# Optimization experiments

Hardware: AMD Instinct MI355X
Metric: run time of the kernel (lower is better)

The kernel has to match this reference:

```python
import math
import jax, jax.numpy as jnp
import numpy as np

D, NH, NL, NP = 256, 8, 4, 4
C = D // NH
VALUE_SHAPES = np.array([[128, 128], [64, 64], [32, 32], [16, 16]], dtype=np.int32)


def _offset_bias():
    # Faithful to MSDeformAttn._reset_parameters grid init for sampling_offsets.bias
    th = np.arange(NH, dtype=np.float32) * (2.0 * np.pi / NH)
    g = np.stack([np.cos(th), np.sin(th)], -1)                      # [NH,2]
    g = g / np.abs(g).max(-1, keepdims=True)
    g = np.tile(g[:, None, None, :], (1, NL, NP, 1))                # [NH,NL,NP,2]
    g = g * np.arange(1, NP + 1, dtype=np.float32)[None, None, :, None]
    return jnp.asarray(g.reshape(-1), jnp.float32)


def setup_inputs() -> dict:
    key = jax.random.key(0)
    ks = jax.random.split(key, 10)
    bs, Q = 8, 2048
    LV = int((VALUE_SHAPES[:, 0] * VALUE_SHAPES[:, 1]).sum())
    s = 0.02
    return {
        "query": jax.random.normal(ks[0], (bs, Q, D), jnp.float32),
        "refer_bbox": jax.random.uniform(ks[1], (bs, Q, NL, 2), jnp.float32),
        "value": jax.random.normal(ks[2], (bs, LV, D), jnp.float32),
        "value_shapes": VALUE_SHAPES,  # static numpy (shapes must be compile-time constants)
        "W_value": jax.random.normal(ks[3], (D, D), jnp.float32) * s,
        "b_value": jnp.zeros((D,), jnp.float32),
        "W_off": jax.random.normal(ks[4], (D, NH * NL * NP * 2), jnp.float32) * 0.01,
        "b_off": _offset_bias(),
        "W_attn": jax.random.normal(ks[5], (D, NH * NL * NP), jnp.float32) * s,
        "b_attn": jnp.zeros((NH * NL * NP,), jnp.float32),
        "W_out": jax.random.normal(ks[6], (D, D), jnp.float32) * s,
        "b_out": jnp.zeros((D,), jnp.float32),
    }


def _ms_deform_attn(value, shapes, loc, attn):
    # value: [bs,LV,NH,C], loc: [bs,Q,NH,NL,NP,2] in [0,1], attn: [bs,Q,NH,NL,NP]
    bs, LV = value.shape[:2]
    Q = loc.shape[1]
    BH = bs * NH
    v = value.transpose(0, 2, 1, 3).reshape(BH, LV, C)              # [BH,LV,C]
    loc = loc.transpose(0, 2, 1, 3, 4, 5).reshape(BH, Q, NL, NP, 2)
    attn = attn.transpose(0, 2, 1, 3, 4).reshape(BH, Q, NL, NP)
    acc = jnp.zeros((BH, Q, C), value.dtype)
    start = 0
    for lvl in range(NL):
        H, W = int(shapes[lvl, 0]), int(shapes[lvl, 1])
        img = v[:, start:start + H * W]                             # [BH,HW,C]
        start += H * W
        # grid_sample(align_corners=False): pixel coord = loc * size - 0.5
        x = loc[:, :, lvl, :, 0] * W - 0.5                          # [BH,Q,NP]
        y = loc[:, :, lvl, :, 1] * H - 0.5
        x0 = jnp.floor(x); y0 = jnp.floor(y)
        fx = x - x0; fy = y - y0
        x0i = x0.astype(jnp.int32); y0i = y0.astype(jnp.int32)
        samp = jnp.zeros((BH, Q, NP, C), value.dtype)
        for dx, dy in ((0, 0), (1, 0), (0, 1), (1, 1)):
            xi = x0i + dx; yi = y0i + dy
            valid = (xi >= 0) & (xi < W) & (yi >= 0) & (yi < H)     # zero padding
            w = (fx if dx else 1.0 - fx) * (fy if dy else 1.0 - fy)
            w = jnp.where(valid, w, 0.0)
            idx = jnp.clip(yi, 0, H - 1) * W + jnp.clip(xi, 0, W - 1)
            g = jnp.take_along_axis(img, idx.reshape(BH, Q * NP)[..., None], axis=1)
            samp = samp + w[..., None] * g.reshape(BH, Q, NP, C)
        acc = acc + (samp * attn[:, :, lvl, :, None]).sum(2)
    return acc.reshape(bs, NH, Q, C).transpose(0, 2, 1, 3).reshape(bs, Q, D)


def reference(query, refer_bbox, value, value_shapes, W_value, b_value,
              W_off, b_off, W_attn, b_attn, W_out, b_out):
    shapes = np.asarray(value_shapes)  # static
    bs, Q = query.shape[:2]
    LV = value.shape[1]
    v = (value @ W_value + b_value).reshape(bs, LV, NH, C)
    off = (query @ W_off + b_off).reshape(bs, Q, NH, NL, NP, 2)
    attn = jax.nn.softmax((query @ W_attn + b_attn).reshape(bs, Q, NH, NL * NP), -1)
    attn = attn.reshape(bs, Q, NH, NL, NP)
    norm = jnp.asarray(shapes[:, ::-1], query.dtype)                # (W,H) per level
    loc = refer_bbox[:, :, None, :, None, :] + off / norm[None, None, None, :, None, :]
    out = _ms_deform_attn(v, shapes, loc, attn)
    return out @ W_out + b_out
```

## Files before the change

kernel.cpp:

```cpp
#include <hip/hip_runtime.h>
#include <hip/hip_bf16.h>

#define D_MODEL 256
#define NHEAD   8
#define NLVL    4
#define NPTS    4
#define CH      32
#define QTOT    2048
#define BS      8
#define LVTOT   21760
#define KDIM    256

typedef __attribute__((ext_vector_type(8))) short bf16x8;
typedef __attribute__((ext_vector_type(4))) float f32x4;

__device__ inline float bf_lo(unsigned u) { unsigned t = u << 16; float f; __builtin_memcpy(&f, &t, 4); return f; }
__device__ inline float bf_hi(unsigned u) { unsigned t = u & 0xffff0000u; float f; __builtin_memcpy(&f, &t, 4); return f; }
__device__ inline float bfu2f(unsigned short s) { unsigned t = (unsigned)s << 16; float f; __builtin_memcpy(&f, &t, 4); return f; }
__device__ inline unsigned short f2bfu(float f) { __hip_bfloat16 h = __float2bfloat16(f); unsigned short u; __builtin_memcpy(&u, &h, 2); return u; }

#define BK  64
#define LDP 72
#define LDC2 136

__device__ inline void transpose_W_body(const float* __restrict__ W,
                                        __hip_bfloat16* __restrict__ Wt,
                                        int sh, int blk, int tid) {
    int t = blk * 256 + tid;
    int k = t >> sh, n = t & ((1 << sh) - 1);
    Wt[n * 256 + k] = __float2bfloat16(W[(k << sh) + n]);
}

__global__ __launch_bounds__(256)
void convert_all(const float* __restrict__ q, __hip_bfloat16* __restrict__ qb,
                 const float* __restrict__ Wv, __hip_bfloat16* __restrict__ Wtv,
                 const float* __restrict__ Wo, __hip_bfloat16* __restrict__ Wto,
                 const float* __restrict__ Wa, __hip_bfloat16* __restrict__ Wta) {
    const int bid = blockIdx.x;
    const int tid = threadIdx.x;
    if (bid < 4096) {
        int t = bid * 256 + tid;
        float4 f = ((const float4*)q)[t];
        __hip_bfloat16 h4[4] = {__float2bfloat16(f.x), __float2bfloat16(f.y),
                                __float2bfloat16(f.z), __float2bfloat16(f.w)};
        ((uint2*)qb)[t] = *(const uint2*)h4;
    } else if (bid < 4352) {
        transpose_W_body(Wv, Wtv, 8, bid - 4096, tid);
    } else if (bid < 4608) {
        transpose_W_body(Wo, Wto, 8, bid - 4352, tid);
    } else {
        transpose_W_body(Wa, Wta, 7, bid - 4608, tid);
    }
}

__global__ __launch_bounds__(256)
void convert_W(const float* __restrict__ W, __hip_bfloat16* __restrict__ Wt, int sh) {
    int t = blockIdx.x * 256 + threadIdx.x;
    int k = t >> sh, n = t & ((1 << sh) - 1);
    Wt[n * 256 + k] = __float2bfloat16(W[(k << sh) + n]);
}

__device__ void value_gemm_body(char* smem, int bid_v,
                                const float* __restrict__ A,
                                const __hip_bfloat16* __restrict__ Wt,
                                const float* __restrict__ bias,
                                __hip_bfloat16* __restrict__ v) {
    __hip_bfloat16* As = (__hip_bfloat16*)smem;
    __hip_bfloat16* Bs = (__hip_bfloat16*)(smem + 128 * LDP * 2);
    __hip_bfloat16* Cs = (__hip_bfloat16*)smem;

    const int tid  = threadIdx.x;
    const int lane = tid & 63;
    const int wave = tid >> 6;
    const int wr   = wave >> 1;
    const int wc   = wave & 1;
    const int cb      = (bid_v & 1) * 128;
    const int rowBase = (bid_v >> 1) * 128;

    const int m0   = lane & 15;
    const int quad = lane >> 4;

    const int ar = tid >> 4;
    const int ac = tid & 15;
    const int br = tid >> 3;
    const int bc = tid & 7;

    f32x4 acc[4][4] = {};

    for (int kc = 0; kc < KDIM; kc += BK) {
#pragma unroll
        for (int i = 0; i < 8; ++i) {
            const int row = i * 16 + ar;
            float4 f = *(const float4*)(A + (size_t)(rowBase + row) * KDIM + kc + ac * 4);
            __hip_bfloat16 t4[4] = {__float2bfloat16(f.x), __float2bfloat16(f.y),
                                    __float2bfloat16(f.z), __float2bfloat16(f.w)};
            *(uint2*)&As[row * LDP + ac * 4] = *(const uint2*)t4;
        }
#pragma unroll
        for (int i = 0; i < 4; ++i) {
            const int row = i * 32 + br;
            uint4 u = *(const uint4*)(Wt + (size_t)(cb + row) * KDIM + kc + bc * 8);
            *(uint4*)&Bs[row * LDP + bc * 8] = u;
        }
        __syncthreads();

#pragma unroll
        for (int ks = 0; ks < 2; ++ks) {
            bf16x8 af[4], bfv[4];
#pragma unroll
            for (int i = 0; i < 4; ++i)
                af[i] = *(const bf16x8*)&As[(wr * 64 + i * 16 + m0) * LDP + ks * 32 + quad * 8];
#pragma unroll
            for (int j = 0; j < 4; ++j)
                bfv[j] = *(const bf16x8*)&Bs[(wc * 64 + j * 16 + m0) * LDP + ks * 32 + quad * 8];
#pragma unroll
            for (int i = 0; i < 4; ++i)
#pragma unroll
                for (int j = 0; j < 4; ++j)
                    acc[i][j] = __builtin_amdgcn_mfma_f32_16x16x32_bf16(af[i], bfv[j], acc[i][j], 0, 0, 0);
        }
        __syncthreads();
    }

    const int b = rowBase / LVTOT;
    const int pixBase = rowBase - b * LVTOT;
#pragma unroll
    for (int half = 0; half < 2; ++half) {
        if (wr == half) {
#pragma unroll
            for (int j = 0; j < 4; ++j) {
                const int lcol = wc * 64 + j * 16 + m0;
                const float bv = bias[cb + lcol];
#pragma unroll
                for (int i = 0; i < 4; ++i) {
                    const int lrow = i * 16 + quad * 4;
#pragma unroll
                    for (int r = 0; r < 4; ++r)
                        Cs[(lrow + r) * LDC2 + lcol] = __float2bfloat16(acc[i][j][r] + bv);
                }
            }
        }
        __syncthreads();
        char* dst = (char*)v + (size_t)(b * LVTOT + pixBase + half * 64) * 512 + cb * 2;
        const char* src = (const char*)Cs;
#pragma unroll
        for (int itr = 0; itr < 4; ++itr) {
            const int o = itr * 4096 + tid * 16;
            const int row = o >> 8;
            const int c   = o & 255;
            uint4 val = *(const uint4*)(src + row * (LDC2 * 2) + c);
            *(uint4*)(dst + (size_t)row * 512 + c) = val;
        }
        if (half == 0) __syncthreads();
    }
}

__device__ void offattn_gemm_body(char* smem, int bid,
                                  const __hip_bfloat16* __restrict__ A,
                                  const __hip_bfloat16* __restrict__ Wt_oa,
                                  const float* __restrict__ b_off,
                                  const float* __restrict__ b_attn,
                                  float* __restrict__ off_ws,
                                  float* __restrict__ logits_ws) {
    __hip_bfloat16* As = (__hip_bfloat16*)smem;
    __hip_bfloat16* Bs = (__hip_bfloat16*)(smem + 128 * LDP * 2);

    const int tid  = threadIdx.x;
    const int lane = tid & 63;
    const int wave = tid >> 6;
    const int rowBase = (bid & 127) * 128;
    const int cb      = (bid >> 7) * 128;

    const int m0   = lane & 15;
    const int quad = lane >> 4;

    const int br = tid >> 3;
    const int bc = tid & 7;

    f32x4 acc[2][8] = {};

    for (int kc = 0; kc < KDIM; kc += BK) {
#pragma unroll
        for (int i = 0; i < 4; ++i) {
            const int row = i * 32 + br;
            uint4 ua = *(const uint4*)(A     + (size_t)(rowBase + row) * KDIM + kc + bc * 8);
            uint4 ub = *(const uint4*)(Wt_oa + (size_t)(cb + row) * KDIM + kc + bc * 8);
            *(uint4*)&As[row * LDP + bc * 8] = ua;
            *(uint4*)&Bs[row * LDP + bc * 8] = ub;
        }
        __syncthreads();

#pragma unroll
        for (int ks = 0; ks < 2; ++ks) {
            bf16x8 af[2], bfv[8];
#pragma unroll
            for (int i = 0; i < 2; ++i)
                af[i] = *(const bf16x8*)&As[(wave * 32 + i * 16 + m0) * LDP + ks * 32 + quad * 8];
#pragma unroll
            for (int j = 0; j < 8; ++j)
                bfv[j] = *(const bf16x8*)&Bs[(j * 16 + m0) * LDP + ks * 32 + quad * 8];
#pragma unroll
            for (int i = 0; i < 2; ++i)
#pragma unroll
                for (int j = 0; j < 8; ++j)
                    acc[i][j] = __builtin_amdgcn_mfma_f32_16x16x32_bf16(af[i], bfv[j], acc[i][j], 0, 0, 0);
        }
        __syncthreads();
    }

#pragma unroll
    for (int j = 0; j < 8; ++j) {
        const int col = cb + j * 16 + m0;
        const bool isOff = (col < 256);
        const float bv = isOff ? b_off[col] : b_attn[col - 256];
#pragma unroll
        for (int i = 0; i < 2; ++i) {
            const int row0 = rowBase + wave * 32 + i * 16 + quad * 4;
#pragma unroll
            for (int r = 0; r < 4; ++r) {
                const float val = acc[i][j][r] + bv;
                if (isOff) off_ws[(size_t)(row0 + r) * 256 + col] = val;
                else       logits_ws[(size_t)(row0 + r) * 128 + (col - 256)] = val;
            }
        }
    }
}

__global__ __launch_bounds__(256, 2)
void fused_gemms(const float* __restrict__ value,
                 const __hip_bfloat16* __restrict__ Wt_v,
                 const float* __restrict__ b_value,
                 __hip_bfloat16* __restrict__ v_ws,
                 const __hip_bfloat16* __restrict__ q_bf,
                 const __hip_bfloat16* __restrict__ Wt_oa,
                 const float* __restrict__ b_off,
                 const float* __restrict__ b_attn,
                 float* __restrict__ off_ws,
                 float* __restrict__ logits_ws) {
    __shared__ __align__(16) char smem[36864];
    const int bid = blockIdx.x;
    if (bid < 384) {
        offattn_gemm_body(smem, bid, q_bf, Wt_oa, b_off, b_attn, off_ws, logits_ws);
    } else {
        value_gemm_body(smem, bid - 384, value, Wt_v, b_value, v_ws);
    }
}

struct StorePlain {
    float* o;
    int ncol;
    __device__ void operator()(int row, int col, float val) const {
        o[(size_t)row * ncol + col] = val;
    }
};

template <typename Store>
__global__ __launch_bounds__(256, 2)
void gemm_bf16_mfma(const __hip_bfloat16* __restrict__ A,
                    const __hip_bfloat16* __restrict__ Wt,
                    const float* __restrict__ bias, Store store) {
    __shared__ __align__(16) __hip_bfloat16 As[128 * LDP];
    __shared__ __align__(16) __hip_bfloat16 Bs[128 * LDP];

    const int tid  = threadIdx.x;
    const int lane = tid & 63;
    const int wave = tid >> 6;
    const int rowBase = blockIdx.x * 128;
    const int cb = blockIdx.y * 128;

    const int m0   = lane & 15;
    const int quad = lane >> 4;

    const int br = tid >> 3;
    const int bc = tid & 7;

    f32x4 acc[2][8] = {};

    for (int kc = 0; kc < KDIM; kc += BK) {
#pragma unroll
        for (int i = 0; i < 4; ++i) {
            const int row = i * 32 + br;
            uint4 ua = *(const uint4*)(A  + (size_t)(rowBase + row) * KDIM + kc + bc * 8);
            uint4 ub = *(const uint4*)(Wt + (size_t)(cb + row) * KDIM + kc + bc * 8);
            *(uint4*)&As[row * LDP + bc * 8] = ua;
            *(uint4*)&Bs[row * LDP + bc * 8] = ub;
        }
        __syncthreads();

#pragma unroll
        for (int ks = 0; ks < 2; ++ks) {
            bf16x8 af[2], bfv[8];
#pragma unroll
            for (int i = 0; i < 2; ++i)
                af[i] = *(const bf16x8*)&As[(wave * 32 + i * 16 + m0) * LDP + ks * 32 + quad * 8];
#pragma unroll
            for (int j = 0; j < 8; ++j)
                bfv[j] = *(const bf16x8*)&Bs[(j * 16 + m0) * LDP + ks * 32 + quad * 8];
#pragma unroll
            for (int i = 0; i < 2; ++i)
#pragma unroll
                for (int j = 0; j < 8; ++j)
                    acc[i][j] = __builtin_amdgcn_mfma_f32_16x16x32_bf16(af[i], bfv[j], acc[i][j], 0, 0, 0);
        }
        __syncthreads();
    }

#pragma unroll
    for (int j = 0; j < 8; ++j) {
        const int col = cb + j * 16 + m0;
        const float bv = bias[col];
#pragma unroll
        for (int i = 0; i < 2; ++i) {
            const int row0 = rowBase + wave * 32 + i * 16 + quad * 4;
#pragma unroll
            for (int r = 0; r < 4; ++r)
                store(row0 + r, col, acc[i][j][r] + bv);
        }
    }
}

__global__ __launch_bounds__(256)
void sample_kernel(const float* __restrict__ off_ws,
                   const float* __restrict__ logits_ws,
                   const float* __restrict__ bbox,
                   const __hip_bfloat16* __restrict__ v,
                   __hip_bfloat16* __restrict__ acc_bf) {
    __shared__ __align__(16) float off_s[8 * 256];
    __shared__ __align__(16) float attn_s[8 * 128];
    __shared__ float bbox_s[64];
    __shared__ __align__(16) int idx_s[1024 * 4];
    __shared__ __align__(8) unsigned short w_s[1024 * 4];

    const int tid = threadIdx.x;
    const int b = blockIdx.x & 7;
    const int gq0 = b * QTOT + (blockIdx.x >> 3) * 8;

    const float4* osrc = (const float4*)(off_ws + (size_t)gq0 * 256);
    ((float4*)off_s)[tid] = osrc[tid];
    ((float4*)off_s)[tid + 256] = osrc[tid + 256];
    const float4* lsrc = (const float4*)(logits_ws + (size_t)gq0 * 128);
    ((float4*)attn_s)[tid] = lsrc[tid];
    if (tid < 64) bbox_s[tid] = bbox[(size_t)gq0 * 8 + tid];
    __syncthreads();

    if (tid < 64) {
        int qq = tid >> 3, h = tid & 7;
        float* p = attn_s + qq * 128 + h * 16;
        float m = p[0];
#pragma unroll
        for (int i = 1; i < 16; ++i) m = fmaxf(m, p[i]);
        float e[16], s = 0.f;
#pragma unroll
        for (int i = 0; i < 16; ++i) { e[i] = __expf(p[i] - m); s += e[i]; }
        float inv = 1.f / s;
#pragma unroll
        for (int i = 0; i < 16; ++i) p[i] = e[i] * inv;
    }
    __syncthreads();

#pragma unroll
    for (int r = 0; r < 4; ++r) {
        const int tap = tid + r * 256;
        const int qq = tap >> 7, h = (tap >> 4) & 7, l = (tap >> 2) & 3, p = tap & 3;
        const int Wd = 128 >> l;
        const int st = (l == 0) ? 0 : (l == 1) ? 16384 : (l == 2) ? 20480 : 21504;

        const float bx = bbox_s[qq * 8 + l * 2 + 0];
        const float by = bbox_s[qq * 8 + l * 2 + 1];
        const float ox = off_s[qq * 256 + h * 32 + l * 8 + p * 2 + 0];
        const float oy = off_s[qq * 256 + h * 32 + l * 8 + p * 2 + 1];
        const float att = attn_s[qq * 128 + h * 16 + l * 4 + p];

        const float x = bx * (float)Wd + ox - 0.5f;
        const float y = by * (float)Wd + oy - 0.5f;
        const float x0f = floorf(x), y0f = floorf(y);
        const float fx = x - x0f, fy = y - y0f;
        const int x0 = (int)x0f, y0 = (int)y0f;
        const int x1 = x0 + 1, y1 = y0 + 1;
        const bool vx0 = (unsigned)x0 < (unsigned)Wd;
        const bool vx1 = (unsigned)x1 < (unsigned)Wd;
        const bool vy0 = (unsigned)y0 < (unsigned)Wd;
        const bool vy1 = (unsigned)y1 < (unsigned)Wd;
        const int cx0 = min(max(x0, 0), Wd - 1), cx1 = min(max(x1, 0), Wd - 1);
        const int cy0 = min(max(y0, 0), Wd - 1), cy1 = min(max(y1, 0), Wd - 1);

        int4 idx;
        idx.x = (st + cy0 * Wd + cx0) << 9;
        idx.y = (st + cy0 * Wd + cx1) << 9;
        idx.z = (st + cy1 * Wd + cx0) << 9;
        idx.w = (st + cy1 * Wd + cx1) << 9;
        float w0 = (vx0 && vy0) ? (1.f - fx) * (1.f - fy) * att : 0.f;
        float w1 = (vx1 && vy0) ? fx * (1.f - fy) * att : 0.f;
        float w2 = (vx0 && vy1) ? (1.f - fx) * fy * att : 0.f;
        float w3 = (vx1 && vy1) ? fx * fy * att : 0.f;

        *(int4*)&idx_s[tap * 4] = idx;
        unsigned short w4[4] = {f2bfu(w0), f2bfu(w1), f2bfu(w2), f2bfu(w3)};
        *(uint2*)&w_s[tap * 4] = *(const uint2*)w4;
    }
    __syncthreads();

    const int lane = tid & 63;
    const int wave = tid >> 6;
    const int g = lane >> 4;
    const int c2 = lane & 15;

    const char* vbase = (const char*)v + (size_t)b * LVTOT * 512 + c2 * 4;

    for (int i = 0; i < 16; ++i) {
        const int pair = wave * 16 + i;
        const int qq = pair >> 3, hh = pair & 7;
        const char* slab = vbase + hh * 64;
        const int tbase = qq * 128 + hh * 16;

        float ax0 = 0.f, ay0 = 0.f, ax1 = 0.f, ay1 = 0.f, ax2 = 0.f, ay2 = 0.f, ax3 = 0.f, ay3 = 0.f;
#pragma unroll
        for (int ts = 0; ts < 4; ++ts) {
            const int tap = tbase + ts * 4 + g;
            const int4 idx = *(const int4*)&idx_s[tap * 4];
            const ushort4 ww = *(const ushort4*)&w_s[tap * 4];
            unsigned u0 = *(const unsigned*)(slab + idx.x);
            unsigned u1 = *(const unsigned*)(slab + idx.y);
            unsigned u2 = *(const unsigned*)(slab + idx.z);
            unsigned u3 = *(const unsigned*)(slab + idx.w);
            float w0 = bfu2f(ww.x), w1 = bfu2f(ww.y), w2 = bfu2f(ww.z), w3 = bfu2f(ww.w);
            ax0 += w0 * bf_lo(u0); ay0 += w0 * bf_hi(u0);
            ax1 += w1 * bf_lo(u1); ay1 += w1 * bf_hi(u1);
            ax2 += w2 * bf_lo(u2); ay2 += w2 * bf_hi(u2);
            ax3 += w3 * bf_lo(u3); ay3 += w3 * bf_hi(u3);
        }
        float sx = (ax0 + ax1) + (ax2 + ax3);
        float sy = (ay0 + ay1) + (ay2 + ay3);
        sx += __shfl_xor(sx, 16); sy += __shfl_xor(sy, 16);
        sx += __shfl_xor(sx, 32); sy += __shfl_xor(sy, 32);
        if (g == 0) {
            __hip_bfloat16 h2[2] = {__float2bfloat16(sx), __float2bfloat16(sy)};
            unsigned packed; __builtin_memcpy(&packed, h2, 4);
            *(unsigned*)((char*)acc_bf + ((size_t)(gq0 + qq) * 256 + hh * 32 + c2 * 2) * 2) = packed;
        }
    }
}

extern "C" void kernel_launch(void* const* d_in, const int* in_sizes, int n_in,
                              void* d_out, int out_size, void* d_ws, size_t ws_size,
                              hipStream_t stream) {
    const float* query   = (const float*)d_in[0];
    const float* bbox    = (const float*)d_in[1];
    const float* value   = (const float*)d_in[2];
    const float* W_value = (const float*)d_in[4];
    const float* b_value = (const float*)d_in[5];
    const float* W_off   = (const float*)d_in[6];
    const float* b_off   = (const float*)d_in[7];
    const float* W_attn  = (const float*)d_in[8];
    const float* b_attn  = (const float*)d_in[9];
    const float* W_out   = (const float*)d_in[10];
    const float* b_out   = (const float*)d_in[11];
    float* out = (float*)d_out;

    char* ws = (char*)d_ws;
    __hip_bfloat16* v_ws  = (__hip_bfloat16*)ws;
    float* off_ws         = (float*)(ws + 89128960);
    float* logits_ws      = (float*)(ws + 89128960 + 16777216);
    __hip_bfloat16* acc_bf = (__hip_bfloat16*)(ws + 89128960 + 16777216 + 8388608);
    __hip_bfloat16* q_bf   = (__hip_bfloat16*)(ws + 89128960 + 16777216 + 8388608 + 8388608);

    __hip_bfloat16* Wt_v    = acc_bf;
    __hip_bfloat16* Wt_off  = acc_bf + 65536;
    __hip_bfloat16* Wt_attn = acc_bf + 131072;
    __hip_bfloat16* Wt_out  = q_bf;

    const int NQ = BS * QTOT;
    const int NVROWS = BS * LVTOT;

    convert_all<<<4736, 256, 0, stream>>>(query, q_bf,
                                          W_value, Wt_v,
                                          W_off, Wt_off,
                                          W_attn, Wt_attn);

    fused_gemms<<<384 + 2 * (NVROWS / 128), 256, 0, stream>>>(
        value, Wt_v, b_value, v_ws,
        q_bf, Wt_off, b_off, b_attn, off_ws, logits_ws);

    convert_W<<<256, 256, 0, stream>>>(W_out, Wt_out, 8);

    sample_kernel<<<NQ / 8, 256, 0, stream>>>(off_ws, logits_ws, bbox, v_ws, acc_bf);

    gemm_bf16_mfma<<<dim3(NQ / 128, 2), 256, 0, stream>>>(
        acc_bf, Wt_out, b_out, StorePlain{out, 256});
}
```

Before: 390.5 us.

## Widen sample gathers to 8-byte loads, compress indices to u16, process two pairs per iteration

In the sampling kernel, each lane now handles four channels with 8-byte gathers instead of two channels with 4-byte gathers. Eight lanes cover a head's 32 channels and eight lane groups cover the 16 taps, so each iteration processes two (query, head) pairs and keeps 16 gathers in flight. Sample indices are stored as 16-bit row indices in shared memory to halve LDS use, and launch bounds request five blocks per CU for occupancy. The cost is more registers per thread, a three-stage shuffle reduction, and relying on LVTOT fitting in 16 bits.

```diff
diff --git a/kernel.cpp b/kernel.cpp
--- a/kernel.cpp
+++ b/kernel.cpp
@@ -319,7 +319,7 @@
     }
 }
 
-__global__ __launch_bounds__(256)
+__global__ __launch_bounds__(256, 5)
 void sample_kernel(const float* __restrict__ off_ws,
                    const float* __restrict__ logits_ws,
                    const float* __restrict__ bbox,
@@ -328,7 +328,7 @@
     __shared__ __align__(16) float off_s[8 * 256];
     __shared__ __align__(16) float attn_s[8 * 128];
     __shared__ float bbox_s[64];
-    __shared__ __align__(16) int idx_s[1024 * 4];
+    __shared__ __align__(8) unsigned short idx_s[1024 * 4];
     __shared__ __align__(8) unsigned short w_s[1024 * 4];
 
     const int tid = threadIdx.x;
@@ -384,17 +384,17 @@
         const int cx0 = min(max(x0, 0), Wd - 1), cx1 = min(max(x1, 0), Wd - 1);
         const int cy0 = min(max(y0, 0), Wd - 1), cy1 = min(max(y1, 0), Wd - 1);
 
-        int4 idx;
-        idx.x = (st + cy0 * Wd + cx0) << 9;
-        idx.y = (st + cy0 * Wd + cx1) << 9;
-        idx.z = (st + cy1 * Wd + cx0) << 9;
-        idx.w = (st + cy1 * Wd + cx1) << 9;
+        unsigned short pi[4];
+        pi[0] = (unsigned short)(st + cy0 * Wd + cx0);
+        pi[1] = (unsigned short)(st + cy0 * Wd + cx1);
+        pi[2] = (unsigned short)(st + cy1 * Wd + cx0);
+        pi[3] = (unsigned short)(st + cy1 * Wd + cx1);
         float w0 = (vx0 && vy0) ? (1.f - fx) * (1.f - fy) * att : 0.f;
         float w1 = (vx1 && vy0) ? fx * (1.f - fy) * att : 0.f;
         float w2 = (vx0 && vy1) ? (1.f - fx) * fy * att : 0.f;
         float w3 = (vx1 && vy1) ? fx * fy * att : 0.f;
 
-        *(int4*)&idx_s[tap * 4] = idx;
+        *(uint2*)&idx_s[tap * 4] = *(const uint2*)pi;
         unsigned short w4[4] = {f2bfu(w0), f2bfu(w1), f2bfu(w2), f2bfu(w3)};
         *(uint2*)&w_s[tap * 4] = *(const uint2*)w4;
     }
@@ -402,41 +402,91 @@
 
     const int lane = tid & 63;
     const int wave = tid >> 6;
-    const int g = lane >> 4;
-    const int c2 = lane & 15;
-
-    const char* vbase = (const char*)v + (size_t)b * LVTOT * 512 + c2 * 4;
-
-    for (int i = 0; i < 16; ++i) {
-        const int pair = wave * 16 + i;
-        const int qq = pair >> 3, hh = pair & 7;
-        const char* slab = vbase + hh * 64;
-        const int tbase = qq * 128 + hh * 16;
-
-        float ax0 = 0.f, ay0 = 0.f, ax1 = 0.f, ay1 = 0.f, ax2 = 0.f, ay2 = 0.f, ax3 = 0.f, ay3 = 0.f;
-#pragma unroll
-        for (int ts = 0; ts < 4; ++ts) {
-            const int tap = tbase + ts * 4 + g;
-            const int4 idx = *(const int4*)&idx_s[tap * 4];
-            const ushort4 ww = *(const ushort4*)&w_s[tap * 4];
-            unsigned u0 = *(const unsigned*)(slab + idx.x);
-            unsigned u1 = *(const unsigned*)(slab + idx.y);
-            unsigned u2 = *(const unsigned*)(slab + idx.z);
-            unsigned u3 = *(const unsigned*)(slab + idx.w);
-            float w0 = bfu2f(ww.x), w1 = bfu2f(ww.y), w2 = bfu2f(ww.z), w3 = bfu2f(ww.w);
-            ax0 += w0 * bf_lo(u0); ay0 += w0 * bf_hi(u0);
-            ax1 += w1 * bf_lo(u1); ay1 += w1 * bf_hi(u1);
-            ax2 += w2 * bf_lo(u2); ay2 += w2 * bf_hi(u2);
-            ax3 += w3 * bf_lo(u3); ay3 += w3 * bf_hi(u3);
-        }
-        float sx = (ax0 + ax1) + (ax2 + ax3);
-        float sy = (ay0 + ay1) + (ay2 + ay3);
-        sx += __shfl_xor(sx, 16); sy += __shfl_xor(sy, 16);
-        sx += __shfl_xor(sx, 32); sy += __shfl_xor(sy, 32);
+    const int g  = lane >> 3;
+    const int c4 = lane & 7;
+
+    const char* vbase = (const char*)v + (size_t)b * LVTOT * 512 + c4 * 8;
+
+    for (int i = 0; i < 8; ++i) {
+        const int pairA = wave * 16 + 2 * i;
+        const int pairB = pairA + 1;
+        const int qqA = pairA >> 3, hhA = pairA & 7;
+        const int qqB = pairB >> 3, hhB = pairB & 7;
+        const char* slabA = vbase + hhA * 64;
+        const char* slabB = vbase + hhB * 64;
+        const int tbA = qqA * 128 + hhA * 16;
+        const int tbB = qqB * 128 + hhB * 16;
+
+        const ushort4 pA0 = *(const ushort4*)&idx_s[(tbA + g) * 4];
+        const ushort4 pA1 = *(const ushort4*)&idx_s[(tbA + 8 + g) * 4];
+        const ushort4 pB0 = *(const ushort4*)&idx_s[(tbB + g) * 4];
+        const ushort4 pB1 = *(const ushort4*)&idx_s[(tbB + 8 + g) * 4];
+        const ushort4 wA0 = *(const ushort4*)&w_s[(tbA + g) * 4];
+        const ushort4 wA1 = *(const ushort4*)&w_s[(tbA + 8 + g) * 4];
+        const ushort4 wB0 = *(const ushort4*)&w_s[(tbB + g) * 4];
+        const ushort4 wB1 = *(const ushort4*)&w_s[(tbB + 8 + g) * 4];
+
+        uint2 uA0 = *(const uint2*)(slabA + ((int)pA0.x << 9));
+        uint2 uA1 = *(const uint2*)(slabA + ((int)pA0.y << 9));
+        uint2 uA2 = *(const uint2*)(slabA + ((int)pA0.z << 9));
+        uint2 uA3 = *(const uint2*)(slabA + ((int)pA0.w << 9));
+        uint2 uA4 = *(const uint2*)(slabA + ((int)pA1.x << 9));
+        uint2 uA5 = *(const uint2*)(slabA + ((int)pA1.y << 9));
+        uint2 uA6 = *(const uint2*)(slabA + ((int)pA1.z << 9));
+        uint2 uA7 = *(const uint2*)(slabA + ((int)pA1.w << 9));
+        uint2 uB0 = *(const uint2*)(slabB + ((int)pB0.x << 9));
+        uint2 uB1 = *(const uint2*)(slabB + ((int)pB0.y << 9));
+        uint2 uB2 = *(const uint2*)(slabB + ((int)pB0.z << 9));
+        uint2 uB3 = *(const uint2*)(slabB + ((int)pB0.w << 9));
+        uint2 uB4 = *(const uint2*)(slabB + ((int)pB1.x << 9));
+        uint2 uB5 = *(const uint2*)(slabB + ((int)pB1.y << 9));
+        uint2 uB6 = *(const uint2*)(slabB + ((int)pB1.z << 9));
+        uint2 uB7 = *(const uint2*)(slabB + ((int)pB1.w << 9));
+
+        float a0 = 0.f, a1 = 0.f, a2 = 0.f, a3 = 0.f;
+        float b0 = 0.f, b1 = 0.f, b2 = 0.f, b3 = 0.f;
+        {
+            float w;
+            w = bfu2f(wA0.x); a0 += w * bf_lo(uA0.x); a1 += w * bf_hi(uA0.x); a2 += w * bf_lo(uA0.y); a3 += w * bf_hi(uA0.y);
+            w = bfu2f(wA0.y); a0 += w * bf_lo(uA1.x); a1 += w * bf_hi(uA1.x); a2 += w * bf_lo(uA1.y); a3 += w * bf_hi(uA1.y);
+            w = bfu2f(wA0.z); a0 += w * bf_lo(uA2.x); a1 += w * bf_hi(uA2.x); a2 += w * bf_lo(uA2.y); a3 += w * bf_hi(uA2.y);
+            w = bfu2f(wA0.w); a0 += w * bf_lo(uA3.x); a1 += w * bf_hi(uA3.x); a2 += w * bf_lo(uA3.y); a3 += w * bf_hi(uA3.y);
+            w = bfu2f(wA1.x); a0 += w * bf_lo(uA4.x); a1 += w * bf_hi(uA4.x); a2 += w * bf_lo(uA4.y); a3 += w * bf_hi(uA4.y);
+            w = bfu2f(wA1.y); a0 += w * bf_lo(uA5.x); a1 += w * bf_hi(uA5.x); a2 += w * bf_lo(uA5.y); a3 += w * bf_hi(uA5.y);
+            w = bfu2f(wA1.z); a0 += w * bf_lo(uA6.x); a1 += w * bf_hi(uA6.x); a2 += w * bf_lo(uA6.y); a3 += w * bf_hi(uA6.y);
+            w = bfu2f(wA1.w); a0 += w * bf_lo(uA7.x); a1 += w * bf_hi(uA7.x); a2 += w * bf_lo(uA7.y); a3 += w * bf_hi(uA7.y);
+            w = bfu2f(wB0.x); b0 += w * bf_lo(uB0.x); b1 += w * bf_hi(uB0.x); b2 += w * bf_lo(uB0.y); b3 += w * bf_hi(uB0.y);
+            w = bfu2f(wB0.y); b0 += w * bf_lo(uB1.x); b1 += w * bf_hi(uB1.x); b2 += w * bf_lo(uB1.y); b3 += w * bf_hi(uB1.y);
+            w = bfu2f(wB0.z); b0 += w * bf_lo(uB2.x); b1 += w * bf_hi(uB2.x); b2 += w * bf_lo(uB2.y); b3 += w * bf_hi(uB2.y);
+            w = bfu2f(wB0.w); b0 += w * bf_lo(uB3.x); b1 += w * bf_hi(uB3.x); b2 += w * bf_lo(uB3.y); b3 += w * bf_hi(uB3.y);
+            w = bfu2f(wB1.x); b0 += w * bf_lo(uB4.x); b1 += w * bf_hi(uB4.x); b2 += w * bf_lo(uB4.y); b3 += w * bf_hi(uB4.y);
+            w = bfu2f(wB1.y); b0 += w * bf_lo(uB5.x); b1 += w * bf_hi(uB5.x); b2 += w * bf_lo(uB5.y); b3 += w * bf_hi(uB5.y);
+            w = bfu2f(wB1.z); b0 += w * bf_lo(uB6.x); b1 += w * bf_hi(uB6.x); b2 += w * bf_lo(uB6.y); b3 += w * bf_hi(uB6.y);
+            w = bfu2f(wB1.w); b0 += w * bf_lo(uB7.x); b1 += w * bf_hi(uB7.x); b2 += w * bf_lo(uB7.y); b3 += w * bf_hi(uB7.y);
+        }
+
+        a0 += __shfl_xor(a0, 8);  a1 += __shfl_xor(a1, 8);  a2 += __shfl_xor(a2, 8);  a3 += __shfl_xor(a3, 8);
+        b0 += __shfl_xor(b0, 8);  b1 += __shfl_xor(b1, 8);  b2 += __shfl_xor(b2, 8);  b3 += __shfl_xor(b3, 8);
+        a0 += __shfl_xor(a0, 16); a1 += __shfl_xor(a1, 16); a2 += __shfl_xor(a2, 16); a3 += __shfl_xor(a3, 16);
+        b0 += __shfl_xor(b0, 16); b1 += __shfl_xor(b1, 16); b2 += __shfl_xor(b2, 16); b3 += __shfl_xor(b3, 16);
+        a0 += __shfl_xor(a0, 32); a1 += __shfl_xor(a1, 32); a2 += __shfl_xor(a2, 32); a3 += __shfl_xor(a3, 32);
+        b0 += __shfl_xor(b0, 32); b1 += __shfl_xor(b1, 32); b2 += __shfl_xor(b2, 32); b3 += __shfl_xor(b3, 32);
+
         if (g == 0) {
-            __hip_bfloat16 h2[2] = {__float2bfloat16(sx), __float2bfloat16(sy)};
-            unsigned packed; __builtin_memcpy(&packed, h2, 4);
-            *(unsigned*)((char*)acc_bf + ((size_t)(gq0 + qq) * 256 + hh * 32 + c2 * 2) * 2) = packed;
+            unsigned lo, hi;
+            __hip_bfloat16 h2[2];
+            h2[0] = __float2bfloat16(a0); h2[1] = __float2bfloat16(a1);
+            __builtin_memcpy(&lo, h2, 4);
+            h2[0] = __float2bfloat16(a2); h2[1] = __float2bfloat16(a3);
+            __builtin_memcpy(&hi, h2, 4);
+            uint2 pk; pk.x = lo; pk.y = hi;
+            *(uint2*)((char*)acc_bf + ((size_t)(gq0 + qqA) * 256 + hhA * 32 + c4 * 4) * 2) = pk;
+            h2[0] = __float2bfloat16(b0); h2[1] = __float2bfloat16(b1);
+            __builtin_memcpy(&lo, h2, 4);
+            h2[0] = __float2bfloat16(b2); h2[1] = __float2bfloat16(b3);
+            __builtin_memcpy(&hi, h2, 4);
+            pk.x = lo; pk.y = hi;
+            *(uint2*)((char*)acc_bf + ((size_t)(gq0 + qqB) * 256 + hhB * 32 + c4 * 4) * 2) = pk;
         }
     }
 }
```

After: 393.0 us. About the same (+0.6%).
